# Performance work log

Measured on AMD Instinct MI355X. Metric: run time of the kernel, lower is better.

## Reference

```python
import jax, jax.numpy as jnp
import numpy as np


def setup_inputs() -> dict:
    key = jax.random.key(0)
    P, B, S = 128, 128, 4096
    k1, k2, k3, k4 = jax.random.split(key, 4)
    # SPD inducing Gram K_ii
    A = jax.random.normal(k1, (P, 2 * P), jnp.float32)
    K_ii = A @ A.T / (2.0 * P) + 1e-2 * jnp.eye(P, dtype=jnp.float32)
    # cross-covariances [B, S, P]
    K_ti = jax.random.normal(k2, (B, S, P), jnp.float32) * 0.1
    # diagonal K_t must dominate the quadratic form so the Schur complement is positive
    Kii_inv = jnp.linalg.inv(K_ii)
    qf = jnp.einsum('bsp,pq,bsq->bs', K_ti, Kii_inv, K_ti)
    K_t = qf + jax.random.uniform(k3, (B, S), jnp.float32) + 0.1
    # learned parameters
    V = jax.random.normal(k4, (P, P), jnp.float32) / jnp.sqrt(P) + jnp.eye(P, dtype=jnp.float32)
    latent_Gscale = jnp.zeros((), jnp.float32)
    dof = 128
    return dict(K_ii=K_ii, K_ti=K_ti, K_t=K_t, V=V, latent_Gscale=latent_Gscale, dof=dof)


def reference(K_ii, K_ti, K_t, V, latent_Gscale, dof):
    P = K_ii.shape[0]
    ti = K_ti.reshape(-1, P)          # [N, P]
    tt = K_t.reshape(-1)              # [N]
    # pos_inv via Cholesky (SPD inverse)
    L = jnp.linalg.cholesky(K_ii)
    Kii_inv = jax.scipy.linalg.cho_solve((L, True), jnp.eye(P, dtype=K_ii.dtype))
    A = ti @ Kii_inv                  # Kti_inv_Kii_flat, [N, P]
    ktt_i = tt - jnp.sum(A * ti, -1)  # Schur complement diag
    # G = V V^T / P * exp(scale)
    G = (V @ V.T) / V.shape[1] * jnp.exp(latent_Gscale)
    Gti = A @ G                       # [N, P]
    gt = jnp.sum(Gti * A, -1) + ktt_i
    # objective: -0.5 * dof * (-(logdet G + logdet Kinv) + tr(Kinv G) - P)
    trace_term = jnp.sum(Kii_inv * G.T)
    logdet_G = jnp.linalg.slogdet(G)[1]
    logdet_Kinv = -2.0 * jnp.sum(jnp.log(jnp.diag(L)))
    obj = -0.5 * dof * (-(logdet_G + logdet_Kinv) + trace_term - P)
    Gii = G
    return (Gii, Gti.reshape(K_ti.shape), gt.reshape(K_t.shape), obj)
```

## Files before the change

kernel.cpp:

```cpp
#include <hip/hip_runtime.h>
#include <cstdint>

typedef __attribute__((ext_vector_type(8))) short short8;
typedef __attribute__((ext_vector_type(4))) float f32x4;

__device__ __forceinline__ unsigned short f2bf(float f) {
    uint32_t u = __builtin_bit_cast(uint32_t, f);
    u += 0x7FFFu + ((u >> 16) & 1u);
    return (unsigned short)(u >> 16);
}

#define SG_OFF   16384
#define SM1_OFF  32768
#define SY_OFF   49152
#define SX_OFF   65536

__global__ __launch_bounds__(256) void k0_G(
    const float* __restrict__ V, const float* __restrict__ gs,
    float* __restrict__ out)
{
    float* sG = out + SG_OFF;
    const float egs = expf(gs[0]) * (1.0f / 128.0f);
    const int ty = threadIdx.x >> 5, tx = threadIdx.x & 31;
    const int r = blockIdx.x * 8 + ty;
    const f32x4* V4 = (const f32x4*)V;
    f32x4 acc = {0.f, 0.f, 0.f, 0.f};
    for (int kq = 0; kq < 32; ++kq) {
        const f32x4 vr = V4[r * 32 + kq];
        #pragma unroll
        for (int e = 0; e < 4; ++e) {
            const f32x4 vc = V4[(tx * 4 + e) * 32 + kq];
            acc[e] += vr[0]*vc[0] + vr[1]*vc[1] + vr[2]*vc[2] + vr[3]*vc[3];
        }
    }
    acc *= egs;
    *(f32x4*)&out[r * 128 + tx * 4] = acc;
    *(f32x4*)&sG[r * 128 + tx * 4] = acc;
}

__global__ __launch_bounds__(512) void kB_setup(
    const float* __restrict__ Kii, const int* __restrict__ dofp,
    float* __restrict__ out, char* __restrict__ wsb)
{
    __shared__ float colA[2][128], colB[2][128], rowX[2][128];
    __shared__ float sDk[128], sDg[128], srd_s[128];
    __shared__ float sRed[4], sTr[8], sLd[2], sTrTot;

    const int tid = threadIdx.x;
    const int ty = tid >> 5, tx = tid & 31;
    const int I0 = ty * 8, J0 = tx * 4;
    const float* sG = out + SG_OFF;
    float* sX = out + SX_OFF;

    f32x4 rA[8], rB[8], rX[8];
    #pragma unroll
    for (int r = 0; r < 8; ++r) {
        rA[r] = *(const f32x4*)&Kii[(size_t)(I0 + r) * 128 + J0];
        rB[r] = *(const f32x4*)&sG[(I0 + r) * 128 + J0];
        f32x4 z = {0.f, 0.f, 0.f, 0.f};
        #pragma unroll
        for (int e = 0; e < 4; ++e) z[e] = (I0 + r == J0 + e) ? 1.0f : 0.0f;
        rX[r] = z;
    }
    if (tx == 0) {
        #pragma unroll
        for (int r = 0; r < 8; ++r) { colA[0][I0 + r] = rA[r][0]; colB[0][I0 + r] = rB[r][0]; }
    }
    if (ty == 0) {
        #pragma unroll
        for (int e = 0; e < 4; ++e) rowX[0][J0 + e] = rX[0][e];
    }
    __syncthreads();

    for (int k = 0; k < 127; ++k) {
        const int b = k & 1;
        const float dK = colA[b][k], dG = colB[b][k];
        const float rdK = 1.0f / dK, rdG = 1.0f / dG;
        if (tid == 0) { sDk[k] = dK; sDg[k] = dG; }

        f32x4 caj = *(const f32x4*)&colA[b][J0];
        f32x4 cbj = *(const f32x4*)&colB[b][J0];
        const f32x4 xj = *(const f32x4*)&rowX[b][J0];
        #pragma unroll
        for (int e = 0; e < 4; ++e)
            if (J0 + e <= k) { caj[e] = 0.0f; cbj[e] = 0.0f; }

        f32x4 ca0 = *(const f32x4*)&colA[b][I0];
        f32x4 ca1 = *(const f32x4*)&colA[b][I0 + 4];
        f32x4 cb0 = *(const f32x4*)&colB[b][I0];
        f32x4 cb1 = *(const f32x4*)&colB[b][I0 + 4];
        #pragma unroll
        for (int r = 0; r < 4; ++r) {
            if (I0 + r <= k)     { ca0[r] = 0.0f; cb0[r] = 0.0f; }
            if (I0 + 4 + r <= k) { ca1[r] = 0.0f; cb1[r] = 0.0f; }
        }

        if (I0 + 7 > k) {
            #pragma unroll
            for (int r = 0; r < 8; ++r) {
                const float am = (r < 4) ? ca0[r & 3] : ca1[r & 3];
                const float bm = (r < 4) ? cb0[r & 3] : cb1[r & 3];
                const float fA = am * rdK;
                const float fB = bm * rdG;
                rA[r] -= fA * caj;
                rB[r] -= fB * cbj;
                rX[r] -= fA * xj;
            }
        }

        const int kn = k + 1, bn = kn & 1;
        if (tx == (kn >> 2)) {
            const int es = kn & 3;
            #pragma unroll
            for (int ee = 0; ee < 4; ++ee) if (ee == es) {
                #pragma unroll
                for (int r = 0; r < 8; ++r) {
                    colA[bn][I0 + r] = rA[r][ee];
                    colB[bn][I0 + r] = rB[r][ee];
                }
            }
        }
        if (ty == (kn >> 3)) {
            const int rs = kn & 7;
            #pragma unroll
            for (int rr = 0; rr < 8; ++rr) if (rr == rs) {
                #pragma unroll
                for (int e = 0; e < 4; ++e) rowX[bn][J0 + e] = rX[rr][e];
            }
        }
        __syncthreads();
    }
    if (tid == 511) { sDk[127] = rA[7][3]; sDg[127] = rB[7][3]; }

    #pragma unroll
    for (int r = 0; r < 8; ++r)
        *(f32x4*)&sX[(I0 + r) * 128 + J0] = rX[r];
    __syncthreads();

    if (tid < 128) {
        srd_s[tid] = 1.0f / sDk[tid];
        float lk = logf(sDk[tid]);
        float lg = logf(sDg[tid]);
        #pragma unroll
        for (int o = 32; o > 0; o >>= 1) { lk += __shfl_xor(lk, o, 64); lg += __shfl_xor(lg, o, 64); }
        if ((tid & 63) == 0) { sRed[(tid >> 6) * 2] = lk; sRed[(tid >> 6) * 2 + 1] = lg; }
    }
    __syncthreads();
    if (tid == 0) {
        sLd[0] = sRed[0] + sRed[2];
        sLd[1] = sRed[1] + sRed[3];
    }
    __syncthreads();

    {
        float* sM1 = out + SM1_OFF;
        const float* sXg = sX;
        f32x4 acc[8] = {};
        for (int k = 0; k < 128; ++k) {
            const f32x4 xv = *(const f32x4*)&sXg[k * 128 + tx * 4];
            const float rd = srd_s[k];
            const f32x4 xa0 = *(const f32x4*)&sXg[k * 128 + I0];
            const f32x4 xa1 = *(const f32x4*)&sXg[k * 128 + I0 + 4];
            #pragma unroll
            for (int r = 0; r < 4; ++r) {
                acc[r]     += (xa0[r] * rd) * xv;
                acc[r + 4] += (xa1[r] * rd) * xv;
            }
        }
        #pragma unroll
        for (int r = 0; r < 8; ++r)
            *(f32x4*)&sM1[(I0 + r) * 128 + tx * 4] = acc[r];
    }
    __syncthreads();

    {
        const float* sGg = out + SG_OFF;
        const float* sM1 = out + SM1_OFF;
        float* sY = out + SY_OFF;
        const f32x4* M14 = (const f32x4*)sM1;
        f32x4 acc[8] = {};
        for (int m = 0; m < 128; ++m) {
            const f32x4 mv = M14[m * 32 + tx];
            #pragma unroll
            for (int r = 0; r < 8; ++r)
                acc[r] += sGg[(I0 + r) * 128 + m] * mv;
        }
        #pragma unroll
        for (int r = 0; r < 8; ++r) {
            const int c = I0 + r;
            *(f32x4*)&sY[c * 128 + tx * 4] = acc[r];
            const uint32_t lo = (uint32_t)f2bf(acc[r][0]) | ((uint32_t)f2bf(acc[r][1]) << 16);
            const uint32_t hi = (uint32_t)f2bf(acc[r][2]) | ((uint32_t)f2bf(acc[r][3]) << 16);
            const uint32_t byteoff = (uint32_t)((c * 256 + tx * 8) ^ ((c & 7) << 4));
            *(uint2*)(wsb + byteoff) = make_uint2(lo, hi);
        }
        const f32x4* G4 = (const f32x4*)sGg;
        float t = 0.0f;
        #pragma unroll
        for (int i = 0; i < 8; ++i) {
            const int idx = tid + i * 512;
            const f32x4 g = G4[idx], mm = M14[idx];
            t += g[0]*mm[0] + g[1]*mm[1] + g[2]*mm[2] + g[3]*mm[3];
        }
        #pragma unroll
        for (int o = 32; o > 0; o >>= 1) t += __shfl_xor(t, o, 64);
        if ((tid & 63) == 0) sTr[tid >> 6] = t;
    }
    __syncthreads();
    if (tid == 0) {
        float tr = 0.0f;
        #pragma unroll
        for (int i = 0; i < 8; ++i) tr += sTr[i];
        sTrTot = tr;
    }
    __syncthreads();

    {
        const float* sM1 = out + SM1_OFF;
        const float* sY = out + SY_OFF;
        const f32x4* Y4 = (const f32x4*)sY;
        const f32x4* M14 = (const f32x4*)sM1;
        f32x4 acc[8];
        #pragma unroll
        for (int r = 0; r < 8; ++r) acc[r] = -M14[(I0 + r) * 32 + tx];
        for (int m = 0; m < 128; ++m) {
            const f32x4 yv = Y4[m * 32 + tx];
            #pragma unroll
            for (int r = 0; r < 8; ++r)
                acc[r] += sM1[(I0 + r) * 128 + m] * yv;
        }
        #pragma unroll
        for (int r = 0; r < 8; ++r) {
            const int c = I0 + r;
            const uint32_t lo = (uint32_t)f2bf(acc[r][0]) | ((uint32_t)f2bf(acc[r][1]) << 16);
            const uint32_t hi = (uint32_t)f2bf(acc[r][2]) | ((uint32_t)f2bf(acc[r][3]) << 16);
            const uint32_t byteoff = (uint32_t)((c * 256 + tx * 8) ^ ((c & 7) << 4));
            *(uint2*)(wsb + 32768 + byteoff) = make_uint2(lo, hi);
        }
    }
    if (tid == 0) {
        const float ldK = sLd[0], ldG = sLd[1];
        const float dof = (float)dofp[0];
        out[67649536] = -0.5f * dof * (-(ldG - ldK) + sTrTot - 128.0f);
    }
}

__global__ __launch_bounds__(512) void main_kernel(
    const float* __restrict__ Kti, const float* __restrict__ Kt,
    const float* __restrict__ ws, float* __restrict__ Gti,
    float* __restrict__ gt)
{
    __shared__ __align__(16) char smem[65536];
    const int tid = threadIdx.x;
    const int lane = tid & 63, wid = tid >> 6;
    const int l15 = lane & 15, l4 = lane >> 4;
    const int brow = blockIdx.x * 256;
    const int wrow = wid * 32;

    const float* tbase = Kti + (size_t)(brow + wrow + l15) * 128;

    f32x4 t[4][4];
    #pragma unroll
    for (int kc = 0; kc < 4; ++kc) {
        const float* p0 = tbase + kc * 32 + l4 * 8;
        const float* p1 = p0 + 16 * 128;
        t[kc][0] = *(const f32x4*)p0;
        t[kc][1] = *(const f32x4*)(p0 + 4);
        t[kc][2] = *(const f32x4*)p1;
        t[kc][3] = *(const f32x4*)(p1 + 4);
    }

    {
        f32x4* s4 = (f32x4*)smem;
        const f32x4* w4 = (const f32x4*)ws;
        #pragma unroll
        for (int i = 0; i < 8; ++i) s4[tid + i * 512] = w4[tid + i * 512];
    }

    short8 a[4][2];
    #pragma unroll
    for (int kc = 0; kc < 4; ++kc) {
        a[kc][0] = { (short)f2bf(t[kc][0][0]), (short)f2bf(t[kc][0][1]), (short)f2bf(t[kc][0][2]), (short)f2bf(t[kc][0][3]),
                     (short)f2bf(t[kc][1][0]), (short)f2bf(t[kc][1][1]), (short)f2bf(t[kc][1][2]), (short)f2bf(t[kc][1][3]) };
        a[kc][1] = { (short)f2bf(t[kc][2][0]), (short)f2bf(t[kc][2][1]), (short)f2bf(t[kc][2][2]), (short)f2bf(t[kc][2][3]),
                     (short)f2bf(t[kc][3][0]), (short)f2bf(t[kc][3][1]), (short)f2bf(t[kc][3][2]), (short)f2bf(t[kc][3][3]) };
    }
    __syncthreads();

    f32x4 accW[2][8] = {};
    f32x4 accZ[2][8] = {};
    #pragma unroll
    for (int kc = 0; kc < 4; ++kc) {
        const int k0 = kc * 32 + l4 * 8;
        #pragma unroll
        for (int ct = 0; ct < 8; ++ct) {
            const int c = ct * 16 + l15;
            const int byteoff = (c * 256 + k0 * 2) ^ ((c & 7) << 4);
            const short8 bW = *(const short8*)(smem + byteoff);
            const short8 bQ = *(const short8*)(smem + 32768 + byteoff);
            accW[0][ct] = __builtin_amdgcn_mfma_f32_16x16x32_bf16(a[kc][0], bW, accW[0][ct], 0, 0, 0);
            accW[1][ct] = __builtin_amdgcn_mfma_f32_16x16x32_bf16(a[kc][1], bW, accW[1][ct], 0, 0, 0);
            accZ[0][ct] = __builtin_amdgcn_mfma_f32_16x16x32_bf16(a[kc][0], bQ, accZ[0][ct], 0, 0, 0);
            accZ[1][ct] = __builtin_amdgcn_mfma_f32_16x16x32_bf16(a[kc][1], bQ, accZ[1][ct], 0, 0, 0);
        }
    }

    #pragma unroll
    for (int rt = 0; rt < 2; ++rt) {
        #pragma unroll
        for (int r = 0; r < 4; ++r) {
            const int row = brow + wrow + rt * 16 + l4 * 4 + r;
            const float* trow = Kti + (size_t)row * 128;
            float p = 0.0f;
            #pragma unroll
            for (int ct = 0; ct < 8; ++ct) p += accZ[rt][ct][r] * trow[ct * 16 + l15];
            p += __shfl_xor(p, 1, 64);
            p += __shfl_xor(p, 2, 64);
            p += __shfl_xor(p, 4, 64);
            p += __shfl_xor(p, 8, 64);
            if (l15 == 0) gt[row] = Kt[row] + p;
        }
    }

    #pragma unroll
    for (int rt = 0; rt < 2; ++rt) {
        #pragma unroll
        for (int r = 0; r < 4; ++r) {
            float* grow = Gti + (size_t)(brow + wrow + rt * 16 + l4 * 4 + r) * 128 + l15;
            #pragma unroll
            for (int ct = 0; ct < 8; ++ct)
                grow[ct * 16] = accW[rt][ct][r];
        }
    }
}

extern "C" void kernel_launch(void* const* d_in, const int* in_sizes, int n_in,
                              void* d_out, int out_size, void* d_ws, size_t ws_size,
                              hipStream_t stream)
{
    const float* Kii = (const float*)d_in[0];
    const float* Kti = (const float*)d_in[1];
    const float* Kt  = (const float*)d_in[2];
    const float* V   = (const float*)d_in[3];
    const float* gs  = (const float*)d_in[4];
    const int*   dof = (const int*)d_in[5];
    float* out = (float*)d_out;
    float* ws  = (float*)d_ws;

    const int N = in_sizes[2];
    const int nblocks = N / 256;

    k0_G<<<16, 256, 0, stream>>>(V, gs, out);
    kB_setup<<<1, 512, 0, stream>>>(Kii, dof, out, (char*)ws);
    main_kernel<<<nblocks, 512, 0, stream>>>(Kti, Kt, ws,
                                             out + 16384,
                                             out + 67125248);
}
```

Baseline: 372.9 us.

## Fuse G computation into setup kernel and stage setup matmuls through LDS

Folds the separate V·Vᵀ kernel into the single-block setup kernel, which removes one launch and the inter-kernel dependency. The intermediate matrices X, M1 and Y are now kept in registers and staged through padded shared-memory tiles instead of being round-tripped through global scratch in the output buffer. The cost is that the G matmul now runs on one block instead of sixteen, and the kernel adds more barriers and shared-memory use. The main kernel dominates runtime, so the overall effect is likely small.

```diff
diff --git a/kernel.cpp b/kernel.cpp
--- a/kernel.cpp
+++ b/kernel.cpp
@@ -10,53 +10,52 @@
     return (unsigned short)(u >> 16);
 }
 
-#define SG_OFF   16384
-#define SM1_OFF  32768
-#define SY_OFF   49152
-#define SX_OFF   65536
-
-__global__ __launch_bounds__(256) void k0_G(
-    const float* __restrict__ V, const float* __restrict__ gs,
-    float* __restrict__ out)
-{
-    float* sG = out + SG_OFF;
-    const float egs = expf(gs[0]) * (1.0f / 128.0f);
-    const int ty = threadIdx.x >> 5, tx = threadIdx.x & 31;
-    const int r = blockIdx.x * 8 + ty;
-    const f32x4* V4 = (const f32x4*)V;
-    f32x4 acc = {0.f, 0.f, 0.f, 0.f};
-    for (int kq = 0; kq < 32; ++kq) {
-        const f32x4 vr = V4[r * 32 + kq];
-        #pragma unroll
-        for (int e = 0; e < 4; ++e) {
-            const f32x4 vc = V4[(tx * 4 + e) * 32 + kq];
-            acc[e] += vr[0]*vc[0] + vr[1]*vc[1] + vr[2]*vc[2] + vr[3]*vc[3];
-        }
-    }
-    acc *= egs;
-    *(f32x4*)&out[r * 128 + tx * 4] = acc;
-    *(f32x4*)&sG[r * 128 + tx * 4] = acc;
-}
-
-__global__ __launch_bounds__(512) void kB_setup(
-    const float* __restrict__ Kii, const int* __restrict__ dofp,
+
+__global__ __launch_bounds__(512, 2) void kS_setup(
+    const float* __restrict__ Kii, const float* __restrict__ V,
+    const float* __restrict__ gscale, const int* __restrict__ dofp,
     float* __restrict__ out, char* __restrict__ wsb)
 {
     __shared__ float colA[2][128], colB[2][128], rowX[2][128];
-    __shared__ float sDk[128], sDg[128], srd_s[128];
-    __shared__ float sRed[4], sTr[8], sLd[2], sTrTot;
+    __shared__ float sDk[128], sDg[128], srd[128];
+    __shared__ float sRed[4], sTr[8];
+    __shared__ float SBIG[8448];
+    __shared__ float SMED[4224];
 
     const int tid = threadIdx.x;
     const int ty = tid >> 5, tx = tid & 31;
     const int I0 = ty * 8, J0 = tx * 4;
-    const float* sG = out + SG_OFF;
-    float* sX = out + SX_OFF;
-
-    f32x4 rA[8], rB[8], rX[8];
+
+    f32x4 rB[8];
+    {
+        const float egs = expf(gscale[0]) * (1.0f / 128.0f);
+        const f32x4* V4 = (const f32x4*)V;
+        float acc[8][4] = {};
+        for (int q = 0; q < 32; ++q) {
+            f32x4 vc[4];
+            #pragma unroll
+            for (int e = 0; e < 4; ++e) vc[e] = V4[(J0 + e) * 32 + q];
+            #pragma unroll
+            for (int r = 0; r < 8; ++r) {
+                const f32x4 vr = V4[(I0 + r) * 32 + q];
+                #pragma unroll
+                for (int e = 0; e < 4; ++e)
+                    acc[r][e] += vr[0]*vc[e][0] + vr[1]*vc[e][1]
+                               + vr[2]*vc[e][2] + vr[3]*vc[e][3];
+            }
+        }
+        #pragma unroll
+        for (int r = 0; r < 8; ++r) {
+            const f32x4 g = { acc[r][0]*egs, acc[r][1]*egs, acc[r][2]*egs, acc[r][3]*egs };
+            rB[r] = g;
+            *(f32x4*)&out[(I0 + r) * 128 + J0] = g;
+        }
+    }
+
+    f32x4 rA[8], rX[8];
     #pragma unroll
     for (int r = 0; r < 8; ++r) {
         rA[r] = *(const f32x4*)&Kii[(size_t)(I0 + r) * 128 + J0];
-        rB[r] = *(const f32x4*)&sG[(I0 + r) * 128 + J0];
         f32x4 z = {0.f, 0.f, 0.f, 0.f};
         #pragma unroll
         for (int e = 0; e < 4; ++e) z[e] = (I0 + r == J0 + e) ? 1.0f : 0.0f;
@@ -131,117 +130,129 @@
         __syncthreads();
     }
     if (tid == 511) { sDk[127] = rA[7][3]; sDg[127] = rB[7][3]; }
-
-    #pragma unroll
-    for (int r = 0; r < 8; ++r)
-        *(f32x4*)&sX[(I0 + r) * 128 + J0] = rX[r];
     __syncthreads();
 
     if (tid < 128) {
-        srd_s[tid] = 1.0f / sDk[tid];
+        srd[tid] = 1.0f / sDk[tid];
         float lk = logf(sDk[tid]);
         float lg = logf(sDg[tid]);
         #pragma unroll
         for (int o = 32; o > 0; o >>= 1) { lk += __shfl_xor(lk, o, 64); lg += __shfl_xor(lg, o, 64); }
         if ((tid & 63) == 0) { sRed[(tid >> 6) * 2] = lk; sRed[(tid >> 6) * 2 + 1] = lg; }
     }
+
+    f32x4 rM1[8] = {};
+    for (int kb = 0; kb < 128; kb += 64) {
+        __syncthreads();
+        if (I0 >= kb && I0 < kb + 64) {
+            #pragma unroll
+            for (int r = 0; r < 8; ++r)
+                *(f32x4*)&SBIG[(I0 - kb + r) * 132 + J0] = rX[r];
+        }
+        __syncthreads();
+        for (int k = 0; k < 64; ++k) {
+            const float rd = srd[kb + k];
+            const f32x4 xa0 = *(const f32x4*)&SBIG[k * 132 + I0];
+            const f32x4 xa1 = *(const f32x4*)&SBIG[k * 132 + I0 + 4];
+            f32x4 xb = *(const f32x4*)&SBIG[k * 132 + J0];
+            xb *= rd;
+            #pragma unroll
+            for (int r = 0; r < 4; ++r) {
+                rM1[r]     += xa0[r] * xb;
+                rM1[r + 4] += xa1[r] * xb;
+            }
+        }
+    }
+
+    {
+        float tr = 0.0f;
+        #pragma unroll
+        for (int r = 0; r < 8; ++r) {
+            const f32x4 g = *(const f32x4*)&out[(I0 + r) * 128 + J0];
+            tr += rM1[r][0]*g[0] + rM1[r][1]*g[1] + rM1[r][2]*g[2] + rM1[r][3]*g[3];
+        }
+        #pragma unroll
+        for (int o = 32; o > 0; o >>= 1) tr += __shfl_xor(tr, o, 64);
+        if ((tid & 63) == 0) sTr[tid >> 6] = tr;
+    }
+
+    f32x4 rY[8] = {};
+    for (int mb = 0; mb < 128; mb += 32) {
+        __syncthreads();
+        for (int v = tid; v < 1024; v += 512) {
+            const int row = v >> 3, c4 = (v & 7) * 4;
+            const f32x4 g = *(const f32x4*)&out[row * 128 + mb + c4];
+            SBIG[row * 36 + c4 + 0] = g[0];
+            SBIG[row * 36 + c4 + 1] = g[1];
+            SBIG[row * 36 + c4 + 2] = g[2];
+            SBIG[row * 36 + c4 + 3] = g[3];
+        }
+        if (I0 >= mb && I0 < mb + 32) {
+            #pragma unroll
+            for (int r = 0; r < 8; ++r)
+                *(f32x4*)&SMED[(I0 - mb + r) * 132 + J0] = rM1[r];
+        }
+        __syncthreads();
+        for (int mm = 0; mm < 32; ++mm) {
+            const f32x4 m1r = *(const f32x4*)&SMED[mm * 132 + J0];
+            #pragma unroll
+            for (int r = 0; r < 8; ++r)
+                rY[r] += SBIG[(I0 + r) * 36 + mm] * m1r;
+        }
+    }
+    #pragma unroll
+    for (int r = 0; r < 8; ++r) {
+        const int c = I0 + r;
+        const uint32_t lo = (uint32_t)f2bf(rY[r][0]) | ((uint32_t)f2bf(rY[r][1]) << 16);
+        const uint32_t hi = (uint32_t)f2bf(rY[r][2]) | ((uint32_t)f2bf(rY[r][3]) << 16);
+        const uint32_t byteoff = (uint32_t)((c * 256 + J0 * 2) ^ ((c & 7) << 4));
+        *(uint2*)(wsb + byteoff) = make_uint2(lo, hi);
+    }
+
+    f32x4 rQ[8];
+    #pragma unroll
+    for (int r = 0; r < 8; ++r) rQ[r] = -rM1[r];
+    for (int mb = 0; mb < 128; mb += 32) {
+        __syncthreads();
+        if (J0 >= mb && J0 < mb + 32) {
+            #pragma unroll
+            for (int r = 0; r < 8; ++r) {
+                #pragma unroll
+                for (int e = 0; e < 4; ++e)
+                    SBIG[(I0 + r) * 36 + (J0 - mb) + e] = rM1[r][e];
+            }
+        }
+        if (I0 >= mb && I0 < mb + 32) {
+            #pragma unroll
+            for (int r = 0; r < 8; ++r)
+                *(f32x4*)&SMED[(I0 - mb + r) * 132 + J0] = rY[r];
+        }
+        __syncthreads();
+        for (int mm = 0; mm < 32; ++mm) {
+            const f32x4 yr = *(const f32x4*)&SMED[mm * 132 + J0];
+            #pragma unroll
+            for (int r = 0; r < 8; ++r)
+                rQ[r] += SBIG[(I0 + r) * 36 + mm] * yr;
+        }
+    }
+    #pragma unroll
+    for (int r = 0; r < 8; ++r) {
+        const int c = I0 + r;
+        const uint32_t lo = (uint32_t)f2bf(rQ[r][0]) | ((uint32_t)f2bf(rQ[r][1]) << 16);
+        const uint32_t hi = (uint32_t)f2bf(rQ[r][2]) | ((uint32_t)f2bf(rQ[r][3]) << 16);
+        const uint32_t byteoff = (uint32_t)((c * 256 + J0 * 2) ^ ((c & 7) << 4));
+        *(uint2*)(wsb + 32768 + byteoff) = make_uint2(lo, hi);
+    }
+
     __syncthreads();
     if (tid == 0) {
-        sLd[0] = sRed[0] + sRed[2];
-        sLd[1] = sRed[1] + sRed[3];
-    }
-    __syncthreads();
-
-    {
-        float* sM1 = out + SM1_OFF;
-        const float* sXg = sX;
-        f32x4 acc[8] = {};
-        for (int k = 0; k < 128; ++k) {
-            const f32x4 xv = *(const f32x4*)&sXg[k * 128 + tx * 4];
-            const float rd = srd_s[k];
-            const f32x4 xa0 = *(const f32x4*)&sXg[k * 128 + I0];
-            const f32x4 xa1 = *(const f32x4*)&sXg[k * 128 + I0 + 4];
-            #pragma unroll
-            for (int r = 0; r < 4; ++r) {
-                acc[r]     += (xa0[r] * rd) * xv;
-                acc[r + 4] += (xa1[r] * rd) * xv;
-            }
-        }
-        #pragma unroll
-        for (int r = 0; r < 8; ++r)
-            *(f32x4*)&sM1[(I0 + r) * 128 + tx * 4] = acc[r];
-    }
-    __syncthreads();
-
-    {
-        const float* sGg = out + SG_OFF;
-        const float* sM1 = out + SM1_OFF;
-        float* sY = out + SY_OFF;
-        const f32x4* M14 = (const f32x4*)sM1;
-        f32x4 acc[8] = {};
-        for (int m = 0; m < 128; ++m) {
-            const f32x4 mv = M14[m * 32 + tx];
-            #pragma unroll
-            for (int r = 0; r < 8; ++r)
-                acc[r] += sGg[(I0 + r) * 128 + m] * mv;
-        }
-        #pragma unroll
-        for (int r = 0; r < 8; ++r) {
-            const int c = I0 + r;
-            *(f32x4*)&sY[c * 128 + tx * 4] = acc[r];
-            const uint32_t lo = (uint32_t)f2bf(acc[r][0]) | ((uint32_t)f2bf(acc[r][1]) << 16);
-            const uint32_t hi = (uint32_t)f2bf(acc[r][2]) | ((uint32_t)f2bf(acc[r][3]) << 16);
-            const uint32_t byteoff = (uint32_t)((c * 256 + tx * 8) ^ ((c & 7) << 4));
-            *(uint2*)(wsb + byteoff) = make_uint2(lo, hi);
-        }
-        const f32x4* G4 = (const f32x4*)sGg;
-        float t = 0.0f;
-        #pragma unroll
-        for (int i = 0; i < 8; ++i) {
-            const int idx = tid + i * 512;
-            const f32x4 g = G4[idx], mm = M14[idx];
-            t += g[0]*mm[0] + g[1]*mm[1] + g[2]*mm[2] + g[3]*mm[3];
-        }
-        #pragma unroll
-        for (int o = 32; o > 0; o >>= 1) t += __shfl_xor(t, o, 64);
-        if ((tid & 63) == 0) sTr[tid >> 6] = t;
-    }
-    __syncthreads();
-    if (tid == 0) {
-        float tr = 0.0f;
-        #pragma unroll
-        for (int i = 0; i < 8; ++i) tr += sTr[i];
-        sTrTot = tr;
-    }
-    __syncthreads();
-
-    {
-        const float* sM1 = out + SM1_OFF;
-        const float* sY = out + SY_OFF;
-        const f32x4* Y4 = (const f32x4*)sY;
-        const f32x4* M14 = (const f32x4*)sM1;
-        f32x4 acc[8];
-        #pragma unroll
-        for (int r = 0; r < 8; ++r) acc[r] = -M14[(I0 + r) * 32 + tx];
-        for (int m = 0; m < 128; ++m) {
-            const f32x4 yv = Y4[m * 32 + tx];
-            #pragma unroll
-            for (int r = 0; r < 8; ++r)
-                acc[r] += sM1[(I0 + r) * 128 + m] * yv;
-        }
-        #pragma unroll
-        for (int r = 0; r < 8; ++r) {
-            const int c = I0 + r;
-            const uint32_t lo = (uint32_t)f2bf(acc[r][0]) | ((uint32_t)f2bf(acc[r][1]) << 16);
-            const uint32_t hi = (uint32_t)f2bf(acc[r][2]) | ((uint32_t)f2bf(acc[r][3]) << 16);
-            const uint32_t byteoff = (uint32_t)((c * 256 + tx * 8) ^ ((c & 7) << 4));
-            *(uint2*)(wsb + 32768 + byteoff) = make_uint2(lo, hi);
-        }
-    }
-    if (tid == 0) {
-        const float ldK = sLd[0], ldG = sLd[1];
+        float trace = 0.0f;
+        #pragma unroll
+        for (int i = 0; i < 8; ++i) trace += sTr[i];
+        const float ldK = sRed[0] + sRed[2];
+        const float ldG = sRed[1] + sRed[3];
         const float dof = (float)dofp[0];
-        out[67649536] = -0.5f * dof * (-(ldG - ldK) + sTrTot - 128.0f);
+        out[67649536] = -0.5f * dof * (-(ldG - ldK) + trace - 128.0f);
     }
 }
 
@@ -350,8 +361,7 @@
     const int N = in_sizes[2];
     const int nblocks = N / 256;
 
-    k0_G<<<16, 256, 0, stream>>>(V, gs, out);
-    kB_setup<<<1, 512, 0, stream>>>(Kii, dof, out, (char*)ws);
+    kS_setup<<<1, 512, 0, stream>>>(Kii, V, gs, dof, out, (char*)ws);
     main_kernel<<<nblocks, 512, 0, stream>>>(Kti, Kt, ws,
                                              out + 16384,
                                              out + 67125248);
```

Result: slower. 592.2 us (+58.8%).
